# Kernel optimization log

Hardware: AMD Instinct MI355X
Metric: run time of the kernel (lower is better)

The kernel has to match this reference:

```python
import jax, jax.numpy as jnp
import numpy as np

N_NODES = 100000


def gcn_conv(x, src, dst, W, b):
    """PyG GCNConv: add self-loops, symmetric deg^-1/2 normalization, W x, scatter-add, bias."""
    n = x.shape[0]
    ones = jnp.ones(src.shape, dtype=x.dtype)
    deg = jax.ops.segment_sum(ones, dst, num_segments=n)  # in-degree incl. self-loops
    dis = jnp.where(deg > 0, jax.lax.rsqrt(deg), 0.0)     # deg^{-1/2}
    norm = dis[src] * dis[dst]                            # [E+N]
    xw = x @ W                                            # transform first: [N, out]
    msg = xw[src] * norm[:, None]                         # gather + scale: [E+N, out]
    out = jax.ops.segment_sum(msg, dst, num_segments=n)   # scatter-add
    return out + b


def setup_inputs() -> dict:
    key = jax.random.key(0)
    k1, k2, k3, k4 = jax.random.split(key, 4)
    N, E, F, H, C = N_NODES, 1600000, 256, 64, 32
    x = jax.random.normal(k1, (N, F), dtype=jnp.float32)
    edge_index = jax.random.randint(k2, (2, E), 0, N, dtype=jnp.int64)
    W1 = jax.random.normal(k3, (F, H), dtype=jnp.float32) * (1.0 / np.sqrt(F))
    b1 = jnp.zeros((H,), dtype=jnp.float32)
    W2 = jax.random.normal(k4, (H, C), dtype=jnp.float32) * (1.0 / np.sqrt(H))
    b2 = jnp.zeros((C,), dtype=jnp.float32)
    return {"x": x, "edge_index": edge_index, "W1": W1, "b1": b1, "W2": W2, "b2": b2}


def reference(x, edge_index, W1, b1, W2, b2):
    n = x.shape[0]
    loop = jnp.arange(n, dtype=edge_index.dtype)
    src = jnp.concatenate([edge_index[0], loop])  # add self-loops once, reuse for both layers
    dst = jnp.concatenate([edge_index[1], loop])
    h = gcn_conv(x, src, dst, W1, b1)
    h = jax.nn.relu(h)
    out = gcn_conv(h, src, dst, W2, b2)
    return out
```

## Files before the change

### kernel.cpp

```cpp
#include <hip/hip_runtime.h>
#include <hip/hip_bf16.h>

static constexpr int F1 = 256;
static constexpr int H1 = 64;
static constexpr int C2 = 32;
static constexpr int BSH2 = 8;
static constexpr int NBLK = 128;

typedef __attribute__((ext_vector_type(8))) short short8;
typedef __attribute__((ext_vector_type(4))) float f32x4;
typedef __attribute__((ext_vector_type(4))) unsigned short ushort4v;

__device__ __forceinline__ unsigned short f2b(float f) {
  __hip_bfloat16 h = __float2bfloat16(f);
  unsigned short u;
  __builtin_memcpy(&u, &h, 2);
  return u;
}
__device__ __forceinline__ float b2f(unsigned short u) {
  return __uint_as_float(((unsigned)u) << 16);
}

__device__ __forceinline__ int ld_src(const int* __restrict__ ei, int E, int e, bool is64) {
  return is64 ? ei[2 * (size_t)e] : ei[e];
}
__device__ __forceinline__ int ld_dst(const int* __restrict__ ei, int E, int e, bool is64) {
  return is64 ? ei[2 * ((size_t)E + (size_t)e)] : ei[(size_t)E + (size_t)e];
}

__device__ __forceinline__ bool detect64(const int* __restrict__ ei, int tid,
                                         int* s_is64) {
  if (tid == 0) *s_is64 = 1;
  __syncthreads();
  int nz = 0;
  for (int i = tid; i < 2048; i += 256) nz |= (ei[2 * i + 1] != 0);
  if (nz) *s_is64 = 0;
  __syncthreads();
  return *s_is64 != 0;
}

__global__ __launch_bounds__(256) void k_wconv(const float* __restrict__ W1,
                                               const float* __restrict__ W2,
                                               unsigned short* __restrict__ wbt1,
                                               unsigned short* __restrict__ wbt2) {
  int tid = blockIdx.x * 256 + threadIdx.x;
  if (tid < 64 * 256) {
    int c = tid >> 8, k = tid & 255;
    wbt1[tid] = f2b(W1[k * 64 + c]);
  }
  if (tid < 32 * 64) {
    int c = tid >> 6, k = tid & 63;
    wbt2[tid] = f2b(W2[k * 32 + c]);
  }
}

__global__ __launch_bounds__(256) void k_partA(const int* __restrict__ ei, int E,
                                               unsigned* __restrict__ gcnt,
                                               unsigned* __restrict__ counter,
                                               int nb, int chunk) {
  __shared__ unsigned lhist[512];
  __shared__ int s_is64;
  if (blockIdx.x == 0 && threadIdx.x == 0) counter[0] = 0;
  const bool is64 = detect64(ei, threadIdx.x, &s_is64);
  const int base = blockIdx.x * chunk;
  const int end = min(E, base + chunk);
  for (int i = threadIdx.x; i < nb; i += 256) lhist[i] = 0;
  __syncthreads();
  for (int e = base + threadIdx.x; e < end; e += 256) {
    int d = ld_dst(ei, E, e, is64);
    atomicAdd(&lhist[d >> BSH2], 1u);
  }
  __syncthreads();
  unsigned* g = gcnt + (size_t)blockIdx.x * nb;
  for (int i = threadIdx.x; i < nb; i += 256) g[i] = lhist[i];
}

__global__ __launch_bounds__(128) void k_bscan(unsigned* __restrict__ gcnt,
                                               unsigned* __restrict__ bcnt,
                                               unsigned* __restrict__ bo,
                                               unsigned* __restrict__ counter,
                                               int nb) {
  __shared__ unsigned ws;
  __shared__ int isLast;
  const int b = blockIdx.x;
  const int t = threadIdx.x;
  unsigned v = gcnt[(size_t)t * nb + b];
  unsigned s = v;
#pragma unroll
  for (int o = 1; o < 64; o <<= 1) {
    unsigned u = __shfl_up(s, o, 64);
    if ((t & 63) >= o) s += u;
  }
  if (t == 63) ws = s;
  __syncthreads();
  if (t >= 64) s += ws;
  gcnt[(size_t)t * nb + b] = s - v;
  if (t == 127) bcnt[b] = s;
  __syncthreads();
  __threadfence();
  if (t == 0) isLast = (atomicAdd(counter, 1u) == (unsigned)(nb - 1));
  __syncthreads();
  if (!isLast) return;
  __threadfence();
  __shared__ unsigned ws2;
  unsigned l[4];
  unsigned lsum = 0;
#pragma unroll
  for (int j = 0; j < 4; ++j) {
    int g = t * 4 + j;
    l[j] = (g < nb) ? bcnt[g] : 0u;
    lsum += l[j];
  }
  unsigned sc = lsum;
#pragma unroll
  for (int o = 1; o < 64; o <<= 1) {
    unsigned u = __shfl_up(sc, o, 64);
    if ((t & 63) >= o) sc += u;
  }
  if (t == 63) ws2 = sc;
  __syncthreads();
  if (t >= 64) sc += ws2;
  unsigned prefix = sc - lsum;
#pragma unroll
  for (int j = 0; j < 4; ++j) {
    int g = t * 4 + j;
    if (g < nb) bo[g] = prefix;
    prefix += l[j];
  }
  if (t == 0) counter[0] = 0;
}

__global__ __launch_bounds__(256) void k_partB(const int* __restrict__ ei, int E,
                                               const unsigned* __restrict__ bo,
                                               const unsigned* __restrict__ gcnt,
                                               unsigned* __restrict__ ebuf,
                                               int nb, int chunk) {
  __shared__ unsigned gb[512];
  __shared__ int s_is64;
  const bool is64 = detect64(ei, threadIdx.x, &s_is64);
  const int base = blockIdx.x * chunk;
  const int end = min(E, base + chunk);
  const unsigned* g = gcnt + (size_t)blockIdx.x * nb;
  for (int i = threadIdx.x; i < nb; i += 256) gb[i] = bo[i] + g[i];
  __syncthreads();
  for (int e = base + threadIdx.x; e < end; e += 256) {
    int s = ld_src(ei, E, e, is64);
    int d = ld_dst(ei, E, e, is64);
    unsigned pos = atomicAdd(&gb[d >> BSH2], 1u);
    ebuf[pos] = ((unsigned)(d & 255) << 24) | (unsigned)s;
  }
}

__global__ __launch_bounds__(256) void k_bucket_csr(const unsigned* __restrict__ bo,
                                                    const unsigned* __restrict__ ebuf,
                                                    int nb, int n, int E,
                                                    unsigned* __restrict__ off,
                                                    float* __restrict__ dis,
                                                    int* __restrict__ srcbin) {
  __shared__ unsigned ldeg[256], loff[256], wsum[4];
  const int b = blockIdx.x;
  const int tid = threadIdx.x;
  const int node0 = b << BSH2;
  const int nn = min(256, n - node0);
  const unsigned beg = bo[b];
  const unsigned end = (b + 1 < nb) ? bo[b + 1] : (unsigned)E;

  ldeg[tid] = 0;
  __syncthreads();
  for (unsigned p = beg + tid; p < end; p += 256) {
    atomicAdd(&ldeg[ebuf[p] >> 24], 1u);
  }
  __syncthreads();
  unsigned v = ldeg[tid];
  unsigned s = v;
#pragma unroll
  for (int o = 1; o < 64; o <<= 1) {
    unsigned t = __shfl_up(s, o, 64);
    if ((tid & 63) >= o) s += t;
  }
  if ((tid & 63) == 63) wsum[tid >> 6] = s;
  __syncthreads();
  unsigned add = 0;
  for (int w = 0; w < (tid >> 6); ++w) add += wsum[w];
  s += add;
  loff[tid] = s - v;
  if (tid < nn) {
    off[node0 + tid] = beg + (s - v);
    dis[node0 + tid] = 1.0f / sqrtf((float)(v + 1u));
  }
  ldeg[tid] = 0;
  __syncthreads();
  for (unsigned p = beg + tid; p < end; p += 256) {
    unsigned e = ebuf[p];
    unsigned li = e >> 24;
    unsigned pos = loff[li] + atomicAdd(&ldeg[li], 1u);
    srcbin[beg + pos] = (int)(e & 0xFFFFFFu);
  }
}

__global__ __launch_bounds__(256) void k_gemm1(const float* __restrict__ x,
                                               const unsigned short* __restrict__ wbt,
                                               const float* __restrict__ dis,
                                               unsigned short* __restrict__ y,
                                               int n) {
  const int tid = threadIdx.x;
  const int wq = tid >> 6, l = tid & 63;
  const int lr = l & 15, lk = l >> 4;
  const int r0 = blockIdx.x * 128 + wq * 32;
  if (r0 >= n) return;

  f32x4 acc[2][4] = {};
  const float* xr0 = x + (size_t)(r0 + lr) * F1;
  const float* xr1 = xr0 + (size_t)16 * F1;
#pragma unroll
  for (int kc = 0; kc < 8; ++kc) {
    const int kb = kc * 32 + lk * 8;
    float4 p0 = *reinterpret_cast<const float4*>(xr0 + kb);
    float4 p1 = *reinterpret_cast<const float4*>(xr0 + kb + 4);
    float4 q0 = *reinterpret_cast<const float4*>(xr1 + kb);
    float4 q1 = *reinterpret_cast<const float4*>(xr1 + kb + 4);
    short8 a0, a1;
    a0[0] = f2b(p0.x); a0[1] = f2b(p0.y); a0[2] = f2b(p0.z); a0[3] = f2b(p0.w);
    a0[4] = f2b(p1.x); a0[5] = f2b(p1.y); a0[6] = f2b(p1.z); a0[7] = f2b(p1.w);
    a1[0] = f2b(q0.x); a1[1] = f2b(q0.y); a1[2] = f2b(q0.z); a1[3] = f2b(q0.w);
    a1[4] = f2b(q1.x); a1[5] = f2b(q1.y); a1[6] = f2b(q1.z); a1[7] = f2b(q1.w);
#pragma unroll
    for (int nt = 0; nt < 4; ++nt) {
      short8 bb = *reinterpret_cast<const short8*>(wbt + (size_t)(nt * 16 + lr) * F1 + kb);
      acc[0][nt] = __builtin_amdgcn_mfma_f32_16x16x32_bf16(a0, bb, acc[0][nt], 0, 0, 0);
      acc[1][nt] = __builtin_amdgcn_mfma_f32_16x16x32_bf16(a1, bb, acc[1][nt], 0, 0, 0);
    }
  }
  float dsc0[4], dsc1[4];
#pragma unroll
  for (int r = 0; r < 4; ++r) {
    dsc0[r] = dis[r0 + lk * 4 + r];
    dsc1[r] = dis[r0 + 16 + lk * 4 + r];
  }
  unsigned short* yb = y + (size_t)r0 * H1;
#pragma unroll
  for (int nt = 0; nt < 4; ++nt)
#pragma unroll
    for (int r = 0; r < 4; ++r) {
      yb[(size_t)(lk * 4 + r) * H1 + nt * 16 + lr] = f2b(acc[0][nt][r] * dsc0[r]);
      yb[(size_t)(16 + lk * 4 + r) * H1 + nt * 16 + lr] = f2b(acc[1][nt][r] * dsc1[r]);
    }
}

__global__ __launch_bounds__(256) void k_gather1(const unsigned* __restrict__ off, int n, int E,
                                                 const int* __restrict__ srcbin,
                                                 const float* __restrict__ dis,
                                                 const unsigned short* __restrict__ xw,
                                                 const float* __restrict__ b1,
                                                 unsigned short* __restrict__ h) {
  const int w = blockIdx.x * 4 + (threadIdx.x >> 6);
  if (w >= n) return;
  const int lane = threadIdx.x & 63;
  const int c4 = (lane & 15) * 4;
  const int st = lane >> 4;
  const float dd = dis[w];
  const unsigned beg = off[w];
  const unsigned end = (w + 1 < n) ? off[w + 1] : (unsigned)E;

  float a0 = 0.f, a1 = 0.f, a2 = 0.f, a3 = 0.f;
  float e0 = 0.f, e1 = 0.f, e2 = 0.f, e3 = 0.f;
  if (st == 0) {
    ushort4v u = *reinterpret_cast<const ushort4v*>(xw + (size_t)w * H1 + c4);
    a0 = b2f(u[0]); a1 = b2f(u[1]); a2 = b2f(u[2]); a3 = b2f(u[3]);
  }
  unsigned p = beg + st;
  for (; p + 4 < end; p += 8) {
    int s0 = srcbin[p];
    int s1 = srcbin[p + 4];
    ushort4v u0 = *reinterpret_cast<const ushort4v*>(xw + (size_t)s0 * H1 + c4);
    ushort4v u1 = *reinterpret_cast<const ushort4v*>(xw + (size_t)s1 * H1 + c4);
    a0 += b2f(u0[0]); a1 += b2f(u0[1]); a2 += b2f(u0[2]); a3 += b2f(u0[3]);
    e0 += b2f(u1[0]); e1 += b2f(u1[1]); e2 += b2f(u1[2]); e3 += b2f(u1[3]);
  }
  if (p < end) {
    int s0 = srcbin[p];
    ushort4v u0 = *reinterpret_cast<const ushort4v*>(xw + (size_t)s0 * H1 + c4);
    a0 += b2f(u0[0]); a1 += b2f(u0[1]); a2 += b2f(u0[2]); a3 += b2f(u0[3]);
  }
  a0 += e0; a1 += e1; a2 += e2; a3 += e3;
  a0 += __shfl_xor(a0, 16, 64); a1 += __shfl_xor(a1, 16, 64);
  a2 += __shfl_xor(a2, 16, 64); a3 += __shfl_xor(a3, 16, 64);
  a0 += __shfl_xor(a0, 32, 64); a1 += __shfl_xor(a1, 32, 64);
  a2 += __shfl_xor(a2, 32, 64); a3 += __shfl_xor(a3, 32, 64);
  if (st == 0) {
    float4 bb = *reinterpret_cast<const float4*>(b1 + c4);
    ushort4v hv;
    hv[0] = f2b(fmaxf(fmaf(a0, dd, bb.x), 0.0f));
    hv[1] = f2b(fmaxf(fmaf(a1, dd, bb.y), 0.0f));
    hv[2] = f2b(fmaxf(fmaf(a2, dd, bb.z), 0.0f));
    hv[3] = f2b(fmaxf(fmaf(a3, dd, bb.w), 0.0f));
    *reinterpret_cast<ushort4v*>(h + (size_t)w * H1 + c4) = hv;
  }
}

__global__ __launch_bounds__(256) void k_gemm2(const unsigned short* __restrict__ h,
                                               const unsigned short* __restrict__ wbt,
                                               const float* __restrict__ dis,
                                               unsigned short* __restrict__ y,
                                               int n) {
  const int tid = threadIdx.x;
  const int wq = tid >> 6, l = tid & 63;
  const int lr = l & 15, lk = l >> 4;
  const int r0 = blockIdx.x * 128 + wq * 32;
  if (r0 >= n) return;

  short8 bfrag[2][2];
#pragma unroll
  for (int kc = 0; kc < 2; ++kc)
#pragma unroll
    for (int nt = 0; nt < 2; ++nt)
      bfrag[kc][nt] =
          *reinterpret_cast<const short8*>(wbt + (size_t)(nt * 16 + lr) * H1 + kc * 32 + lk * 8);

  f32x4 acc[2][2] = {};
  const unsigned short* h0 = h + (size_t)(r0 + lr) * H1;
  const unsigned short* h1 = h0 + (size_t)16 * H1;
#pragma unroll
  for (int kc = 0; kc < 2; ++kc) {
    const int kb = kc * 32 + lk * 8;
    short8 a0 = *reinterpret_cast<const short8*>(h0 + kb);
    short8 a1 = *reinterpret_cast<const short8*>(h1 + kb);
#pragma unroll
    for (int nt = 0; nt < 2; ++nt) {
      acc[0][nt] = __builtin_amdgcn_mfma_f32_16x16x32_bf16(a0, bfrag[kc][nt], acc[0][nt], 0, 0, 0);
      acc[1][nt] = __builtin_amdgcn_mfma_f32_16x16x32_bf16(a1, bfrag[kc][nt], acc[1][nt], 0, 0, 0);
    }
  }
  float dsc0[4], dsc1[4];
#pragma unroll
  for (int r = 0; r < 4; ++r) {
    dsc0[r] = dis[r0 + lk * 4 + r];
    dsc1[r] = dis[r0 + 16 + lk * 4 + r];
  }
  unsigned short* yb = y + (size_t)r0 * C2;
#pragma unroll
  for (int nt = 0; nt < 2; ++nt)
#pragma unroll
    for (int r = 0; r < 4; ++r) {
      yb[(size_t)(lk * 4 + r) * C2 + nt * 16 + lr] = f2b(acc[0][nt][r] * dsc0[r]);
      yb[(size_t)(16 + lk * 4 + r) * C2 + nt * 16 + lr] = f2b(acc[1][nt][r] * dsc1[r]);
    }
}

__global__ __launch_bounds__(256) void k_gather2(const unsigned* __restrict__ off, int n, int E,
                                                 const int* __restrict__ srcbin,
                                                 const float* __restrict__ dis,
                                                 const unsigned short* __restrict__ xw,
                                                 const float* __restrict__ b2,
                                                 float* __restrict__ out) {
  const int w = blockIdx.x * 4 + (threadIdx.x >> 6);
  if (w >= n) return;
  const int lane = threadIdx.x & 63;
  const int c4 = (lane & 7) * 4;
  const int st = lane >> 3;
  const float dd = dis[w];
  const unsigned beg = off[w];
  const unsigned end = (w + 1 < n) ? off[w + 1] : (unsigned)E;

  float a0 = 0.f, a1 = 0.f, a2 = 0.f, a3 = 0.f;
  float e0 = 0.f, e1 = 0.f, e2 = 0.f, e3 = 0.f;
  if (st == 0) {
    ushort4v u = *reinterpret_cast<const ushort4v*>(xw + (size_t)w * C2 + c4);
    a0 = b2f(u[0]); a1 = b2f(u[1]); a2 = b2f(u[2]); a3 = b2f(u[3]);
  }
  unsigned p = beg + st;
  for (; p + 8 < end; p += 16) {
    int s0 = srcbin[p];
    int s1 = srcbin[p + 8];
    ushort4v u0 = *reinterpret_cast<const ushort4v*>(xw + (size_t)s0 * C2 + c4);
    ushort4v u1 = *reinterpret_cast<const ushort4v*>(xw + (size_t)s1 * C2 + c4);
    a0 += b2f(u0[0]); a1 += b2f(u0[1]); a2 += b2f(u0[2]); a3 += b2f(u0[3]);
    e0 += b2f(u1[0]); e1 += b2f(u1[1]); e2 += b2f(u1[2]); e3 += b2f(u1[3]);
  }
  if (p < end) {
    int s0 = srcbin[p];
    ushort4v u0 = *reinterpret_cast<const ushort4v*>(xw + (size_t)s0 * C2 + c4);
    a0 += b2f(u0[0]); a1 += b2f(u0[1]); a2 += b2f(u0[2]); a3 += b2f(u0[3]);
  }
  a0 += e0; a1 += e1; a2 += e2; a3 += e3;
  a0 += __shfl_xor(a0, 8, 64);  a1 += __shfl_xor(a1, 8, 64);
  a2 += __shfl_xor(a2, 8, 64);  a3 += __shfl_xor(a3, 8, 64);
  a0 += __shfl_xor(a0, 16, 64); a1 += __shfl_xor(a1, 16, 64);
  a2 += __shfl_xor(a2, 16, 64); a3 += __shfl_xor(a3, 16, 64);
  a0 += __shfl_xor(a0, 32, 64); a1 += __shfl_xor(a1, 32, 64);
  a2 += __shfl_xor(a2, 32, 64); a3 += __shfl_xor(a3, 32, 64);
  if (st == 0) {
    float4 bb = *reinterpret_cast<const float4*>(b2 + c4);
    float4 o;
    o.x = fmaf(a0, dd, bb.x);
    o.y = fmaf(a1, dd, bb.y);
    o.z = fmaf(a2, dd, bb.z);
    o.w = fmaf(a3, dd, bb.w);
    *reinterpret_cast<float4*>(out + (size_t)w * C2 + c4) = o;
  }
}

extern "C" void kernel_launch(void* const* d_in, const int* in_sizes, int n_in,
                              void* d_out, int out_size, void* d_ws, size_t ws_size,
                              hipStream_t stream) {
  const float* x  = (const float*)d_in[0];
  const int*   ei = (const int*)d_in[1];
  const float* W1 = (const float*)d_in[2];
  const float* b1 = (const float*)d_in[3];
  const float* W2 = (const float*)d_in[4];
  const float* b2 = (const float*)d_in[5];
  float* out = (float*)d_out;

  const int n = in_sizes[0] / F1;
  const int E = in_sizes[1] / 2;
  const int nb = (n + 255) >> BSH2;

  char* ws = (char*)d_ws;
  size_t woff = 0;
  auto take = [&](size_t bytes) -> void* {
    void* p = ws + woff;
    woff += (bytes + 255) & ~(size_t)255;
    return p;
  };
  float*          dis     = (float*)take((size_t)n * 4);
  unsigned*       off     = (unsigned*)take((size_t)n * 4);
  unsigned*       bcnt    = (unsigned*)take((size_t)nb * 4);
  unsigned*       bo      = (unsigned*)take((size_t)nb * 4);
  unsigned*       gcnt    = (unsigned*)take((size_t)NBLK * nb * 4);
  unsigned*       counter = (unsigned*)take(256);
  unsigned short* wbt1    = (unsigned short*)take((size_t)H1 * F1 * 2);
  unsigned short* wbt2    = (unsigned short*)take((size_t)C2 * H1 * 2);
  int*            srcbin  = (int*)take((size_t)E * 4);
  char*           big     = (char*)take((size_t)E * 4 > (size_t)n * H1 * 2 ? (size_t)E * 4
                                                                            : (size_t)n * H1 * 2);
  unsigned*       ebuf = (unsigned*)big;
  unsigned short* xw1  = (unsigned short*)big;
  unsigned short* h    = (unsigned short*)take((size_t)n * H1 * 2);
  unsigned short* xw2  = (unsigned short*)take((size_t)n * C2 * 2);
  (void)ws_size;

  const int ntiles = (n + 127) / 128;
  const int chunk = (((E + NBLK - 1) / NBLK) + 255) & ~255;

  k_wconv<<<64, 256, 0, stream>>>(W1, W2, wbt1, wbt2);
  k_partA<<<NBLK, 256, 0, stream>>>(ei, E, gcnt, counter, nb, chunk);
  k_bscan<<<nb, 128, 0, stream>>>(gcnt, bcnt, bo, counter, nb);
  k_partB<<<NBLK, 256, 0, stream>>>(ei, E, bo, gcnt, ebuf, nb, chunk);
  k_bucket_csr<<<nb, 256, 0, stream>>>(bo, ebuf, nb, n, E, off, dis, srcbin);

  k_gemm1<<<ntiles, 256, 0, stream>>>(x, wbt1, dis, xw1, n);
  k_gather1<<<(n + 3) / 4, 256, 0, stream>>>(off, n, E, srcbin, dis, xw1, b1, h);

  k_gemm2<<<ntiles, 256, 0, stream>>>(h, wbt2, dis, xw2, n);
  k_gather2<<<(n + 3) / 4, 256, 0, stream>>>(off, n, E, srcbin, dis, xw2, b2, out);
}
```

Before: 215.2 us.

## Fuse CSR build stages into one persistent kernel with grid barriers

```diff
diff --git a/kernel.cpp b/kernel.cpp
--- a/kernel.cpp
+++ b/kernel.cpp
@@ -28,173 +28,167 @@
   return is64 ? ei[2 * ((size_t)E + (size_t)e)] : ei[(size_t)E + (size_t)e];
 }
 
-__device__ __forceinline__ bool detect64(const int* __restrict__ ei, int tid,
-                                         int* s_is64) {
-  if (tid == 0) *s_is64 = 1;
-  __syncthreads();
-  int nz = 0;
-  for (int i = tid; i < 2048; i += 256) nz |= (ei[2 * i + 1] != 0);
-  if (nz) *s_is64 = 0;
-  __syncthreads();
-  return *s_is64 != 0;
-}
-
-__global__ __launch_bounds__(256) void k_wconv(const float* __restrict__ W1,
-                                               const float* __restrict__ W2,
-                                               unsigned short* __restrict__ wbt1,
-                                               unsigned short* __restrict__ wbt2) {
-  int tid = blockIdx.x * 256 + threadIdx.x;
-  if (tid < 64 * 256) {
-    int c = tid >> 8, k = tid & 255;
-    wbt1[tid] = f2b(W1[k * 64 + c]);
-  }
-  if (tid < 32 * 64) {
-    int c = tid >> 6, k = tid & 63;
-    wbt2[tid] = f2b(W2[k * 32 + c]);
-  }
-}
-
-__global__ __launch_bounds__(256) void k_partA(const int* __restrict__ ei, int E,
-                                               unsigned* __restrict__ gcnt,
-                                               unsigned* __restrict__ counter,
-                                               int nb, int chunk) {
+__device__ __forceinline__ void gsync(unsigned* bar, int idx, unsigned nblk) {
+  __syncthreads();
+  if (threadIdx.x == 0) {
+    __threadfence();
+    unsigned prev = atomicAdd(&bar[idx * 2], 1u);
+    if (prev == nblk - 1u) {
+      atomicExch(&bar[idx * 2 + 1], 1u);
+    } else {
+      while (atomicAdd(&bar[idx * 2 + 1], 0u) == 0u) {
+        __builtin_amdgcn_s_sleep(2);
+      }
+    }
+    __threadfence();
+  }
+  __syncthreads();
+}
+
+__global__ __launch_bounds__(256) void k_csr(const int* __restrict__ ei, int E,
+                                             const float* __restrict__ W1,
+                                             const float* __restrict__ W2,
+                                             unsigned short* __restrict__ wbt1,
+                                             unsigned short* __restrict__ wbt2,
+                                             unsigned* __restrict__ gcnt,
+                                             unsigned* __restrict__ bcnt,
+                                             unsigned* __restrict__ bo,
+                                             unsigned* __restrict__ bar,
+                                             unsigned* __restrict__ ebuf,
+                                             unsigned* __restrict__ off,
+                                             float* __restrict__ dis,
+                                             int* __restrict__ srcbin,
+                                             int nb, int n, int chunk) {
   __shared__ unsigned lhist[512];
+  __shared__ unsigned ldeg[256], loff[256], ts[256];
+  __shared__ unsigned wsum_[4];
   __shared__ int s_is64;
-  if (blockIdx.x == 0 && threadIdx.x == 0) counter[0] = 0;
-  const bool is64 = detect64(ei, threadIdx.x, &s_is64);
-  const int base = blockIdx.x * chunk;
-  const int end = min(E, base + chunk);
-  for (int i = threadIdx.x; i < nb; i += 256) lhist[i] = 0;
-  __syncthreads();
-  for (int e = base + threadIdx.x; e < end; e += 256) {
+  const int tid = threadIdx.x;
+  const int blk = blockIdx.x;
+  const int base = blk * chunk;
+  const int bend = min(E, base + chunk);
+
+  {
+    int gidx = blk * 256 + tid;
+    if (gidx < 64 * 256) {
+      int c = gidx >> 8, k = gidx & 255;
+      wbt1[gidx] = f2b(W1[k * 64 + c]);
+    }
+    int g2 = gidx - 64 * 256;
+    if (g2 >= 0 && g2 < 32 * 64) {
+      int c = g2 >> 6, k = g2 & 63;
+      wbt2[g2] = f2b(W2[k * 32 + c]);
+    }
+  }
+
+  if (tid == 0) s_is64 = 1;
+  __syncthreads();
+  {
+    int nz = 0;
+    for (int i = tid; i < 2048; i += 256) nz |= (ei[2 * i + 1] != 0);
+    if (nz) s_is64 = 0;
+  }
+  __syncthreads();
+  const bool is64 = s_is64 != 0;
+
+  for (int i = tid; i < nb; i += 256) lhist[i] = 0;
+  __syncthreads();
+  for (int e = base + tid; e < bend; e += 256) {
     int d = ld_dst(ei, E, e, is64);
     atomicAdd(&lhist[d >> BSH2], 1u);
   }
   __syncthreads();
-  unsigned* g = gcnt + (size_t)blockIdx.x * nb;
-  for (int i = threadIdx.x; i < nb; i += 256) g[i] = lhist[i];
-}
-
-__global__ __launch_bounds__(128) void k_bscan(unsigned* __restrict__ gcnt,
-                                               unsigned* __restrict__ bcnt,
-                                               unsigned* __restrict__ bo,
-                                               unsigned* __restrict__ counter,
-                                               int nb) {
-  __shared__ unsigned ws;
-  __shared__ int isLast;
-  const int b = blockIdx.x;
-  const int t = threadIdx.x;
-  unsigned v = gcnt[(size_t)t * nb + b];
-  unsigned s = v;
-#pragma unroll
-  for (int o = 1; o < 64; o <<= 1) {
-    unsigned u = __shfl_up(s, o, 64);
-    if ((t & 63) >= o) s += u;
-  }
-  if (t == 63) ws = s;
-  __syncthreads();
-  if (t >= 64) s += ws;
-  gcnt[(size_t)t * nb + b] = s - v;
-  if (t == 127) bcnt[b] = s;
-  __syncthreads();
-  __threadfence();
-  if (t == 0) isLast = (atomicAdd(counter, 1u) == (unsigned)(nb - 1));
-  __syncthreads();
-  if (!isLast) return;
-  __threadfence();
-  __shared__ unsigned ws2;
-  unsigned l[4];
-  unsigned lsum = 0;
-#pragma unroll
-  for (int j = 0; j < 4; ++j) {
-    int g = t * 4 + j;
-    l[j] = (g < nb) ? bcnt[g] : 0u;
-    lsum += l[j];
-  }
-  unsigned sc = lsum;
-#pragma unroll
-  for (int o = 1; o < 64; o <<= 1) {
-    unsigned u = __shfl_up(sc, o, 64);
-    if ((t & 63) >= o) sc += u;
-  }
-  if (t == 63) ws2 = sc;
-  __syncthreads();
-  if (t >= 64) sc += ws2;
-  unsigned prefix = sc - lsum;
-#pragma unroll
-  for (int j = 0; j < 4; ++j) {
-    int g = t * 4 + j;
-    if (g < nb) bo[g] = prefix;
-    prefix += l[j];
-  }
-  if (t == 0) counter[0] = 0;
-}
-
-__global__ __launch_bounds__(256) void k_partB(const int* __restrict__ ei, int E,
-                                               const unsigned* __restrict__ bo,
-                                               const unsigned* __restrict__ gcnt,
-                                               unsigned* __restrict__ ebuf,
-                                               int nb, int chunk) {
-  __shared__ unsigned gb[512];
-  __shared__ int s_is64;
-  const bool is64 = detect64(ei, threadIdx.x, &s_is64);
-  const int base = blockIdx.x * chunk;
-  const int end = min(E, base + chunk);
-  const unsigned* g = gcnt + (size_t)blockIdx.x * nb;
-  for (int i = threadIdx.x; i < nb; i += 256) gb[i] = bo[i] + g[i];
-  __syncthreads();
-  for (int e = base + threadIdx.x; e < end; e += 256) {
+  for (int i = tid; i < nb; i += 256) {
+    unsigned v = lhist[i];
+    gcnt[(size_t)blk * nb + i] = v;
+    if (v) atomicAdd(&bcnt[i], v);
+  }
+  gsync(bar, 0, NBLK);
+
+  {
+    const int iters = (nb + NBLK - 1) / NBLK;
+    for (int it = 0; it < iters; ++it) {
+      int b = blk + it * NBLK;
+      bool act = (tid < NBLK) && (b < nb);
+      unsigned v = act ? gcnt[(size_t)tid * nb + b] : 0u;
+      unsigned s = v;
+#pragma unroll
+      for (int o = 1; o < 64; o <<= 1) {
+        unsigned u = __shfl_up(s, o, 64);
+        if ((tid & 63) >= o) s += u;
+      }
+      if (tid == 63) wsum_[0] = s;
+      __syncthreads();
+      if (act && tid >= 64) s += wsum_[0];
+      if (act) gcnt[(size_t)tid * nb + b] = s - v;
+      __syncthreads();
+    }
+    if (blk == 0) {
+      unsigned l0 = (2 * tid + 0 < nb) ? bcnt[2 * tid + 0] : 0u;
+      unsigned l1 = (2 * tid + 1 < nb) ? bcnt[2 * tid + 1] : 0u;
+      ts[tid] = l0 + l1;
+      __syncthreads();
+      for (int o = 1; o < 256; o <<= 1) {
+        unsigned v = ts[tid];
+        unsigned add = (tid >= o) ? ts[tid - o] : 0u;
+        __syncthreads();
+        ts[tid] = v + add;
+        __syncthreads();
+      }
+      unsigned prefix = (tid > 0) ? ts[tid - 1] : 0u;
+      if (2 * tid + 0 < nb) bo[2 * tid + 0] = prefix;
+      if (2 * tid + 1 < nb) bo[2 * tid + 1] = prefix + l0;
+    }
+  }
+  gsync(bar, 1, NBLK);
+
+  for (int i = tid; i < nb; i += 256) lhist[i] = bo[i] + gcnt[(size_t)blk * nb + i];
+  __syncthreads();
+  for (int e = base + tid; e < bend; e += 256) {
     int s = ld_src(ei, E, e, is64);
     int d = ld_dst(ei, E, e, is64);
-    unsigned pos = atomicAdd(&gb[d >> BSH2], 1u);
+    unsigned pos = atomicAdd(&lhist[d >> BSH2], 1u);
     ebuf[pos] = ((unsigned)(d & 255) << 24) | (unsigned)s;
   }
-}
-
-__global__ __launch_bounds__(256) void k_bucket_csr(const unsigned* __restrict__ bo,
-                                                    const unsigned* __restrict__ ebuf,
-                                                    int nb, int n, int E,
-                                                    unsigned* __restrict__ off,
-                                                    float* __restrict__ dis,
-                                                    int* __restrict__ srcbin) {
-  __shared__ unsigned ldeg[256], loff[256], wsum[4];
-  const int b = blockIdx.x;
-  const int tid = threadIdx.x;
-  const int node0 = b << BSH2;
-  const int nn = min(256, n - node0);
-  const unsigned beg = bo[b];
-  const unsigned end = (b + 1 < nb) ? bo[b + 1] : (unsigned)E;
-
-  ldeg[tid] = 0;
-  __syncthreads();
-  for (unsigned p = beg + tid; p < end; p += 256) {
-    atomicAdd(&ldeg[ebuf[p] >> 24], 1u);
-  }
-  __syncthreads();
-  unsigned v = ldeg[tid];
-  unsigned s = v;
-#pragma unroll
-  for (int o = 1; o < 64; o <<= 1) {
-    unsigned t = __shfl_up(s, o, 64);
-    if ((tid & 63) >= o) s += t;
-  }
-  if ((tid & 63) == 63) wsum[tid >> 6] = s;
-  __syncthreads();
-  unsigned add = 0;
-  for (int w = 0; w < (tid >> 6); ++w) add += wsum[w];
-  s += add;
-  loff[tid] = s - v;
-  if (tid < nn) {
-    off[node0 + tid] = beg + (s - v);
-    dis[node0 + tid] = 1.0f / sqrtf((float)(v + 1u));
-  }
-  ldeg[tid] = 0;
-  __syncthreads();
-  for (unsigned p = beg + tid; p < end; p += 256) {
-    unsigned e = ebuf[p];
-    unsigned li = e >> 24;
-    unsigned pos = loff[li] + atomicAdd(&ldeg[li], 1u);
-    srcbin[beg + pos] = (int)(e & 0xFFFFFFu);
+  gsync(bar, 2, NBLK);
+
+  for (int b = blk; b < nb; b += NBLK) {
+    const int node0 = b << BSH2;
+    const int nn = min(256, n - node0);
+    const unsigned beg = bo[b];
+    const unsigned end = (b + 1 < nb) ? bo[b + 1] : (unsigned)E;
+    ldeg[tid] = 0;
+    __syncthreads();
+    for (unsigned p = beg + tid; p < end; p += 256) {
+      atomicAdd(&ldeg[ebuf[p] >> 24], 1u);
+    }
+    __syncthreads();
+    unsigned v = ldeg[tid];
+    unsigned s = v;
+#pragma unroll
+    for (int o = 1; o < 64; o <<= 1) {
+      unsigned t = __shfl_up(s, o, 64);
+      if ((tid & 63) >= o) s += t;
+    }
+    if ((tid & 63) == 63) wsum_[tid >> 6] = s;
+    __syncthreads();
+    unsigned add = 0;
+    for (int w = 0; w < (tid >> 6); ++w) add += wsum_[w];
+    s += add;
+    loff[tid] = s - v;
+    if (tid < nn) {
+      off[node0 + tid] = beg + (s - v);
+      dis[node0 + tid] = 1.0f / sqrtf((float)(v + 1u));
+    }
+    ldeg[tid] = 0;
+    __syncthreads();
+    for (unsigned p = beg + tid; p < end; p += 256) {
+      unsigned e = ebuf[p];
+      unsigned li = e >> 24;
+      unsigned pos = loff[li] + atomicAdd(&ldeg[li], 1u);
+      srcbin[beg + pos] = (int)(e & 0xFFFFFFu);
+    }
+    __syncthreads();
   }
 }
 
@@ -203,7 +197,15 @@
                                                const float* __restrict__ dis,
                                                unsigned short* __restrict__ y,
                                                int n) {
+  __shared__ __align__(16) unsigned short wl[64][264];
   const int tid = threadIdx.x;
+  for (int i = tid; i < 64 * 32; i += 256) {
+    int row = i >> 5, c8 = (i & 31) * 8;
+    *reinterpret_cast<float4*>(&wl[row][c8]) =
+        *reinterpret_cast<const float4*>(wbt + (size_t)row * F1 + c8);
+  }
+  __syncthreads();
+
   const int wq = tid >> 6, l = tid & 63;
   const int lr = l & 15, lk = l >> 4;
   const int r0 = blockIdx.x * 128 + wq * 32;
@@ -226,7 +228,7 @@
     a1[4] = f2b(q1.x); a1[5] = f2b(q1.y); a1[6] = f2b(q1.z); a1[7] = f2b(q1.w);
 #pragma unroll
     for (int nt = 0; nt < 4; ++nt) {
-      short8 bb = *reinterpret_cast<const short8*>(wbt + (size_t)(nt * 16 + lr) * F1 + kb);
+      short8 bb = *reinterpret_cast<const short8*>(&wl[nt * 16 + lr][kb]);
       acc[0][nt] = __builtin_amdgcn_mfma_f32_16x16x32_bf16(a0, bb, acc[0][nt], 0, 0, 0);
       acc[1][nt] = __builtin_amdgcn_mfma_f32_16x16x32_bf16(a1, bb, acc[1][nt], 0, 0, 0);
     }
@@ -422,17 +424,18 @@
     woff += (bytes + 255) & ~(size_t)255;
     return p;
   };
-  float*          dis     = (float*)take((size_t)n * 4);
-  unsigned*       off     = (unsigned*)take((size_t)n * 4);
-  unsigned*       bcnt    = (unsigned*)take((size_t)nb * 4);
-  unsigned*       bo      = (unsigned*)take((size_t)nb * 4);
-  unsigned*       gcnt    = (unsigned*)take((size_t)NBLK * nb * 4);
-  unsigned*       counter = (unsigned*)take(256);
-  unsigned short* wbt1    = (unsigned short*)take((size_t)H1 * F1 * 2);
-  unsigned short* wbt2    = (unsigned short*)take((size_t)C2 * H1 * 2);
-  int*            srcbin  = (int*)take((size_t)E * 4);
-  char*           big     = (char*)take((size_t)E * 4 > (size_t)n * H1 * 2 ? (size_t)E * 4
-                                                                            : (size_t)n * H1 * 2);
+  float*          dis   = (float*)take((size_t)n * 4);
+  unsigned*       off   = (unsigned*)take((size_t)n * 4);
+  unsigned*       zblk  = (unsigned*)take(32 + (size_t)nb * 4);
+  unsigned*       bar   = zblk;
+  unsigned*       bcnt  = zblk + 8;
+  unsigned*       bo    = (unsigned*)take((size_t)nb * 4);
+  unsigned*       gcnt  = (unsigned*)take((size_t)NBLK * nb * 4);
+  unsigned short* wbt1  = (unsigned short*)take((size_t)H1 * F1 * 2);
+  unsigned short* wbt2  = (unsigned short*)take((size_t)C2 * H1 * 2);
+  int*            srcbin = (int*)take((size_t)E * 4);
+  char*           big   = (char*)take((size_t)E * 4 > (size_t)n * H1 * 2 ? (size_t)E * 4
+                                                                          : (size_t)n * H1 * 2);
   unsigned*       ebuf = (unsigned*)big;
   unsigned short* xw1  = (unsigned short*)big;
   unsigned short* h    = (unsigned short*)take((size_t)n * H1 * 2);
@@ -442,11 +445,9 @@
   const int ntiles = (n + 127) / 128;
   const int chunk = (((E + NBLK - 1) / NBLK) + 255) & ~255;
 
-  k_wconv<<<64, 256, 0, stream>>>(W1, W2, wbt1, wbt2);
-  k_partA<<<NBLK, 256, 0, stream>>>(ei, E, gcnt, counter, nb, chunk);
-  k_bscan<<<nb, 128, 0, stream>>>(gcnt, bcnt, bo, counter, nb);
-  k_partB<<<NBLK, 256, 0, stream>>>(ei, E, bo, gcnt, ebuf, nb, chunk);
-  k_bucket_csr<<<nb, 256, 0, stream>>>(bo, ebuf, nb, n, E, off, dis, srcbin);
+  hipMemsetAsync(zblk, 0, 32 + (size_t)nb * 4, stream);
+  k_csr<<<NBLK, 256, 0, stream>>>(ei, E, W1, W2, wbt1, wbt2, gcnt, bcnt, bo, bar,
+                                  ebuf, off, dis, srcbin, nb, n, chunk);
 
   k_gemm1<<<ntiles, 256, 0, stream>>>(x, wbt1, dis, xw1, n);
   k_gather1<<<(n + 3) / 4, 256, 0, stream>>>(off, n, E, srcbin, dis, xw1, b1, h);
```

New measurement: 238.4 us, median of 5. +10.8%, slower.
